# Kernel tuning notes

Measured on AMD Instinct MI355X. Metric: run time of the kernel, lower is better.

The kernel has to match this reference:

```python
import jax, jax.numpy as jnp
import numpy as np

B, H, L, D = 2, 16, 2048, 64


def setup_inputs() -> dict:
    key = jax.random.key(0)
    kq, kk, kv = jax.random.split(key, 3)
    return {
        "query": jax.random.normal(kq, (B, H, L, D), dtype=jnp.float32),
        "key": jax.random.normal(kk, (B, H, L, D), dtype=jnp.float32),
        "value": jax.random.normal(kv, (B, H, L, D), dtype=jnp.float32),
        "dhead": D,
        "causal": 1,
    }


def reference(query, key, value, dhead, causal):
    # mode='dhead': muP attention with scale 1/dhead (not 1/sqrt(dhead)).
    # Inputs/outputs in [B, H, L, D] layout (the torch code transposes to
    # [B, L, H, D] for the einsum and transposes back; net layout is the same).
    scale = 1.0 / dhead
    a = jnp.einsum('bhld,bhLd->bhlL', query, key) * scale  # [B,H,L,L]
    if causal:
        seq = a.shape[-1]
        mask = jnp.tril(jnp.ones((seq, seq), dtype=bool))  # [L,L]
        a = jnp.where(mask, a, jnp.float32(-jnp.inf))
    a = jax.nn.softmax(a, axis=-1)
    out = jnp.einsum('bhlL,bhLd->bhld', a, value)  # [B,H,L,D]
    return out
```

## Files before the change

### kernel.cpp

```cpp
#include <hip/hip_runtime.h>

#define BHH 32
#define SEQ 2048
#define DH 64
#define BQ 64
#define BK 64
#define NKT (SEQ / BK)
#define NQB (SEQ / BQ)
#define NT  (BHH * NKT)

typedef __attribute__((ext_vector_type(8))) _Float16 half8_t;
typedef __attribute__((ext_vector_type(4))) _Float16 half4_t;
typedef __attribute__((ext_vector_type(2))) _Float16 half2_t;
typedef __attribute__((ext_vector_type(4))) float f32x4;

__device__ __forceinline__ void async_copy16(const void* g, const void* lds) {
    __builtin_amdgcn_global_load_lds(
        (const __attribute__((address_space(1))) unsigned int*)g,
        (__attribute__((address_space(3))) unsigned int*)lds, 16, 0, 0);
}

__device__ __forceinline__ half2_t pkrtz(float a, float b) {
    return __builtin_bit_cast(half2_t, __builtin_amdgcn_cvt_pkrtz(a, b));
}

__global__ __launch_bounds__(256) void prep_kv(const float* __restrict__ K,
                                               const float* __restrict__ V,
                                               _Float16* __restrict__ Kf,
                                               _Float16* __restrict__ Vf) {
    __shared__ _Float16 l[64 * 76];
    const int t = threadIdx.x;
    const int wave = t >> 6, lane = t & 63, ln15 = lane & 15, quad = lane >> 4;
    const int row = t >> 2, col0 = (t & 3) * 16;
    int b = blockIdx.x;

    if (b < NT) {
        const float4* src = (const float4*)(K + (size_t)b * 4096 + row * 64 + col0);
        #pragma unroll
        for (int q = 0; q < 2; ++q) {
            float4 f0 = src[q * 2], f1 = src[q * 2 + 1];
            half8_t w = { (_Float16)f0.x, (_Float16)f0.y, (_Float16)f0.z, (_Float16)f0.w,
                          (_Float16)f1.x, (_Float16)f1.y, (_Float16)f1.z, (_Float16)f1.w };
            *(half8_t*)&l[row * 72 + col0 + q * 8] = w;
        }
        __syncthreads();
        #pragma unroll
        for (int p = 0; p < 2; ++p) {
            const int bid = wave * 2 + p, c = bid >> 1, k0 = bid & 1;
            half8_t w = *(const half8_t*)&l[(c * 16 + ln15) * 72 + k0 * 32 + quad * 8];
            *(half8_t*)&Kf[(size_t)b * 4096 + bid * 512 + lane * 8] = w;
        }
    } else {
        b -= NT;
        const float4* src = (const float4*)(V + (size_t)b * 4096 + row * 64 + col0);
        #pragma unroll
        for (int q = 0; q < 4; ++q) {
            float4 f = src[q];
            half4_t w = { (_Float16)f.x, (_Float16)f.y, (_Float16)f.z, (_Float16)f.w };
            *(half4_t*)&l[row * 76 + col0 + q * 4] = w;
        }
        __syncthreads();
        #pragma unroll
        for (int p = 0; p < 2; ++p) {
            const int f = wave * 2 + p, cn = f >> 1, k1 = f & 1;
            half8_t w;
            #pragma unroll
            for (int jj = 0; jj < 8; ++jj) {
                const int krow = k1 * 32 + ((jj & 4) << 2) + quad * 4 + (jj & 3);
                w[jj] = l[krow * 76 + cn * 16 + ln15];
            }
            *(half8_t*)&Vf[(size_t)b * 4096 + f * 512 + lane * 8] = w;
        }
    }
}

__global__ __launch_bounds__(256, 3) void fattn_kernel(
        const float* __restrict__ Q, const _Float16* __restrict__ Kf,
        const _Float16* __restrict__ Vf, float* __restrict__ O) {
    const int bh = blockIdx.x & 31;
    const int r = blockIdx.x >> 5, j = r & 7, rnd = r >> 3;
    const int qb = (rnd == 0) ? 31 - j : (rnd == 1) ? 16 + j
                 : (rnd == 2) ? 15 - j : j;
    const int tid  = threadIdx.x;
    const int wave = tid >> 6;
    const int lane = tid & 63;
    const int ln15 = lane & 15;
    const int quad = lane >> 4;

    __shared__ _Float16 ldsK[3][4096];
    __shared__ _Float16 ldsV[3][4096];

    const size_t base = (size_t)bh * SEQ * DH;
    const int q0   = qb * BQ;
    const int qrow = q0 + wave * 16;
    const size_t tb = (size_t)(bh * NKT) * 4096;

    const _Float16* gsrc = ((wave < 2) ? Kf : Vf) + tb + (wave & 1) * 2048 + lane * 8;
    _Float16* sdst0 = ((wave < 2) ? &ldsK[0][0] : &ldsV[0][0]) + (wave & 1) * 2048;

    #define STAGE(kt_, dd_) do {                                         \
        const _Float16* s_ = gsrc + (size_t)(kt_) * 4096;                \
        _Float16* d_ = (dd_);                                            \
        async_copy16(s_,        d_);                                     \
        async_copy16(s_ + 512,  d_ + 512);                               \
        async_copy16(s_ + 1024, d_ + 1024);                              \
        async_copy16(s_ + 1536, d_ + 1536);                              \
    } while (0)

    const float qscale = 1.44269504f / 64.0f;
    half8_t qfrag[2];
    {
        const float* qp = Q + base + (size_t)(qrow + ln15) * DH + quad * 8;
        #pragma unroll
        for (int k0 = 0; k0 < 2; ++k0) {
            float4 a = *(const float4*)(qp + k0 * 32);
            float4 b2 = *(const float4*)(qp + k0 * 32 + 4);
            qfrag[k0] = (half8_t){
                (_Float16)(a.x * qscale), (_Float16)(a.y * qscale),
                (_Float16)(a.z * qscale), (_Float16)(a.w * qscale),
                (_Float16)(b2.x * qscale), (_Float16)(b2.y * qscale),
                (_Float16)(b2.z * qscale), (_Float16)(b2.w * qscale) };
        }
    }
    asm volatile("" ::: "memory");

    STAGE(0, sdst0);
    STAGE(1, sdst0 + 4096);

    f32x4 acc[4] = {};
    float l_lane = 0.f;

    const _Float16* kbase = &ldsK[0][0] + lane * 8;
    const _Float16* vbase = &ldsV[0][0] + lane * 8;
    const int myrel = wave * 16 + ln15;
    const int kq4 = quad * 4;

    int bs = 0, b2 = 2;
    for (int kt = 0; kt <= qb; ++kt) {
        if (kt < qb)
            asm volatile("s_waitcnt vmcnt(4) lgkmcnt(0)\n\ts_barrier" ::: "memory");
        else
            asm volatile("s_waitcnt vmcnt(0) lgkmcnt(0)\n\ts_barrier" ::: "memory");

        if (kt + 2 <= qb) STAGE(kt + 2, sdst0 + b2 * 4096);

        const _Float16* kk = kbase + bs * 4096;
        const _Float16* vv = vbase + bs * 4096;

        f32x4 st[4];
        #pragma unroll
        for (int c = 0; c < 4; ++c) {
            half8_t kf0 = *(const half8_t*)(kk + c * 1024);
            half8_t kf1 = *(const half8_t*)(kk + c * 1024 + 512);
            f32x4 a = {};
            a = __builtin_amdgcn_mfma_f32_16x16x32_f16(kf0, qfrag[0], a, 0, 0, 0);
            a = __builtin_amdgcn_mfma_f32_16x16x32_f16(kf1, qfrag[1], a, 0, 0, 0);
            st[c] = a;
        }

        float p[4][4];
        #pragma unroll
        for (int c = 0; c < 4; ++c)
            #pragma unroll
            for (int rr = 0; rr < 4; ++rr)
                p[c][rr] = __builtin_amdgcn_exp2f(st[c][rr]);

        if (kt == qb) {
            #pragma unroll
            for (int c = 0; c < 4; ++c)
                #pragma unroll
                for (int rr = 0; rr < 4; ++rr)
                    if (c * 16 + kq4 + rr > myrel) p[c][rr] = 0.f;
        }

        float s0 = (p[0][0] + p[0][1]) + (p[0][2] + p[0][3]);
        float s1 = (p[1][0] + p[1][1]) + (p[1][2] + p[1][3]);
        float s2 = (p[2][0] + p[2][1]) + (p[2][2] + p[2][3]);
        float s3 = (p[3][0] + p[3][1]) + (p[3][2] + p[3][3]);
        l_lane += (s0 + s1) + (s2 + s3);

        union P8 { half2_t h2[4]; half8_t h8; };
        P8 u0, u1;
        u0.h2[0] = pkrtz(p[0][0], p[0][1]);
        u0.h2[1] = pkrtz(p[0][2], p[0][3]);
        u0.h2[2] = pkrtz(p[1][0], p[1][1]);
        u0.h2[3] = pkrtz(p[1][2], p[1][3]);
        u1.h2[0] = pkrtz(p[2][0], p[2][1]);
        u1.h2[1] = pkrtz(p[2][2], p[2][3]);
        u1.h2[2] = pkrtz(p[3][0], p[3][1]);
        u1.h2[3] = pkrtz(p[3][2], p[3][3]);
        half8_t pb0 = u0.h8, pb1 = u1.h8;

        __builtin_amdgcn_s_setprio(1);
        #pragma unroll
        for (int cn = 0; cn < 4; ++cn) {
            half8_t vf0 = *(const half8_t*)(vv + cn * 1024);
            acc[cn] = __builtin_amdgcn_mfma_f32_16x16x32_f16(vf0, pb0, acc[cn], 0, 0, 0);
            half8_t vf1 = *(const half8_t*)(vv + cn * 1024 + 512);
            acc[cn] = __builtin_amdgcn_mfma_f32_16x16x32_f16(vf1, pb1, acc[cn], 0, 0, 0);
        }
        __builtin_amdgcn_s_setprio(0);

        bs = (bs == 2) ? 0 : bs + 1;
        b2 = (b2 == 2) ? 0 : b2 + 1;
    }

    {
        float l_i = l_lane + __shfl_xor(l_lane, 16);
        l_i += __shfl_xor(l_i, 32);
        const float rl = 1.0f / l_i;
        float* op = O + base + (size_t)(qrow + ln15) * DH;
        #pragma unroll
        for (int cn = 0; cn < 4; ++cn) {
            float4 o;
            o.x = acc[cn][0] * rl;
            o.y = acc[cn][1] * rl;
            o.z = acc[cn][2] * rl;
            o.w = acc[cn][3] * rl;
            *(float4*)(op + cn * 16 + kq4) = o;
        }
    }
    #undef STAGE
}

extern "C" void kernel_launch(void* const* d_in, const int* in_sizes, int n_in,
                              void* d_out, int out_size, void* d_ws, size_t ws_size,
                              hipStream_t stream) {
    const float* Q = (const float*)d_in[0];
    const float* K = (const float*)d_in[1];
    const float* V = (const float*)d_in[2];
    float* O = (float*)d_out;
    _Float16* Kf = (_Float16*)d_ws;
    _Float16* Vf = Kf + (size_t)NT * 4096;
    prep_kv<<<2 * NT, 256, 0, stream>>>(K, V, Kf, Vf);
    fattn_kernel<<<NQB * BHH, 256, 0, stream>>>(Q, Kf, Vf, O);
}
```

Baseline: 122.6 us.

## Software-pipeline QK^T of next tile with softmax and PV of current tile

Restructures the causal attention loop so the QK^T MFMAs for tile kt+1 are issued before the exp/pack/PV work of tile kt, with a prologue computing the first scores and an epilogue that handles the masked diagonal tile. The intent is to let the matrix units overlap the exp2 and conversion work and hide dependency latency. It also moves to a full vmcnt(0) wait each iteration because the K of the next tile must already be resident. The cost is more live registers (stn alongside st) and a shallower effective prefetch, which could reduce occupancy or expose load latency.

```diff
diff --git a/kernel.cpp b/kernel.cpp
--- a/kernel.cpp
+++ b/kernel.cpp
@@ -126,6 +126,7 @@
 
     STAGE(0, sdst0);
     STAGE(1, sdst0 + 4096);
+    asm volatile("s_waitcnt vmcnt(0) lgkmcnt(0)\n\ts_barrier" ::: "memory");
 
     f32x4 acc[4] = {};
     float l_lane = 0.f;
@@ -135,27 +136,37 @@
     const int myrel = wave * 16 + ln15;
     const int kq4 = quad * 4;
 
-    int bs = 0, b2 = 2;
-    for (int kt = 0; kt <= qb; ++kt) {
-        if (kt < qb)
-            asm volatile("s_waitcnt vmcnt(4) lgkmcnt(0)\n\ts_barrier" ::: "memory");
-        else
+    f32x4 st[4];
+    #pragma unroll
+    for (int c = 0; c < 4; ++c) {
+        half8_t kf0 = *(const half8_t*)(kbase + c * 1024);
+        half8_t kf1 = *(const half8_t*)(kbase + c * 1024 + 512);
+        f32x4 a = {};
+        a = __builtin_amdgcn_mfma_f32_16x16x32_f16(kf0, qfrag[0], a, 0, 0, 0);
+        a = __builtin_amdgcn_mfma_f32_16x16x32_f16(kf1, qfrag[1], a, 0, 0, 0);
+        st[c] = a;
+    }
+
+    union P8 { half2_t h2[4]; half8_t h8; };
+    int rv = 0, rk = 1, sb = 2;
+
+    for (int kt = 0; kt < qb; ++kt) {
+        if (kt)
             asm volatile("s_waitcnt vmcnt(0) lgkmcnt(0)\n\ts_barrier" ::: "memory");
-
-        if (kt + 2 <= qb) STAGE(kt + 2, sdst0 + b2 * 4096);
-
-        const _Float16* kk = kbase + bs * 4096;
-        const _Float16* vv = vbase + bs * 4096;
-
-        f32x4 st[4];
-        #pragma unroll
-        for (int c = 0; c < 4; ++c) {
-            half8_t kf0 = *(const half8_t*)(kk + c * 1024);
-            half8_t kf1 = *(const half8_t*)(kk + c * 1024 + 512);
-            f32x4 a = {};
-            a = __builtin_amdgcn_mfma_f32_16x16x32_f16(kf0, qfrag[0], a, 0, 0, 0);
-            a = __builtin_amdgcn_mfma_f32_16x16x32_f16(kf1, qfrag[1], a, 0, 0, 0);
-            st[c] = a;
+        if (kt + 2 <= qb) STAGE(kt + 2, sdst0 + sb * 4096);
+
+        f32x4 stn[4];
+        {
+            const _Float16* kk = kbase + rk * 4096;
+            #pragma unroll
+            for (int c = 0; c < 4; ++c) {
+                half8_t kf0 = *(const half8_t*)(kk + c * 1024);
+                half8_t kf1 = *(const half8_t*)(kk + c * 1024 + 512);
+                f32x4 a = {};
+                a = __builtin_amdgcn_mfma_f32_16x16x32_f16(kf0, qfrag[0], a, 0, 0, 0);
+                a = __builtin_amdgcn_mfma_f32_16x16x32_f16(kf1, qfrag[1], a, 0, 0, 0);
+                stn[c] = a;
+            }
         }
 
         float p[4][4];
@@ -165,21 +176,6 @@
             for (int rr = 0; rr < 4; ++rr)
                 p[c][rr] = __builtin_amdgcn_exp2f(st[c][rr]);
 
-        if (kt == qb) {
-            #pragma unroll
-            for (int c = 0; c < 4; ++c)
-                #pragma unroll
-                for (int rr = 0; rr < 4; ++rr)
-                    if (c * 16 + kq4 + rr > myrel) p[c][rr] = 0.f;
-        }
-
-        float s0 = (p[0][0] + p[0][1]) + (p[0][2] + p[0][3]);
-        float s1 = (p[1][0] + p[1][1]) + (p[1][2] + p[1][3]);
-        float s2 = (p[2][0] + p[2][1]) + (p[2][2] + p[2][3]);
-        float s3 = (p[3][0] + p[3][1]) + (p[3][2] + p[3][3]);
-        l_lane += (s0 + s1) + (s2 + s3);
-
-        union P8 { half2_t h2[4]; half8_t h8; };
         P8 u0, u1;
         u0.h2[0] = pkrtz(p[0][0], p[0][1]);
         u0.h2[1] = pkrtz(p[0][2], p[0][3]);
@@ -191,6 +187,58 @@
         u1.h2[3] = pkrtz(p[3][2], p[3][3]);
         half8_t pb0 = u0.h8, pb1 = u1.h8;
 
+        {
+            const _Float16* vv = vbase + rv * 4096;
+            __builtin_amdgcn_s_setprio(1);
+            #pragma unroll
+            for (int cn = 0; cn < 4; ++cn) {
+                half8_t vf0 = *(const half8_t*)(vv + cn * 1024);
+                acc[cn] = __builtin_amdgcn_mfma_f32_16x16x32_f16(vf0, pb0, acc[cn], 0, 0, 0);
+                half8_t vf1 = *(const half8_t*)(vv + cn * 1024 + 512);
+                acc[cn] = __builtin_amdgcn_mfma_f32_16x16x32_f16(vf1, pb1, acc[cn], 0, 0, 0);
+            }
+            __builtin_amdgcn_s_setprio(0);
+        }
+
+        float s0 = (p[0][0] + p[0][1]) + (p[0][2] + p[0][3]);
+        float s1 = (p[1][0] + p[1][1]) + (p[1][2] + p[1][3]);
+        float s2 = (p[2][0] + p[2][1]) + (p[2][2] + p[2][3]);
+        float s3 = (p[3][0] + p[3][1]) + (p[3][2] + p[3][3]);
+        l_lane += (s0 + s1) + (s2 + s3);
+
+        #pragma unroll
+        for (int c = 0; c < 4; ++c) st[c] = stn[c];
+        rv = (rv == 2) ? 0 : rv + 1;
+        rk = (rk == 2) ? 0 : rk + 1;
+        sb = (sb == 2) ? 0 : sb + 1;
+    }
+
+    {
+        if (qb)
+            asm volatile("s_waitcnt vmcnt(0) lgkmcnt(0)\n\ts_barrier" ::: "memory");
+
+        float p[4][4];
+        #pragma unroll
+        for (int c = 0; c < 4; ++c)
+            #pragma unroll
+            for (int rr = 0; rr < 4; ++rr) {
+                float v = __builtin_amdgcn_exp2f(st[c][rr]);
+                if (c * 16 + kq4 + rr > myrel) v = 0.f;
+                p[c][rr] = v;
+            }
+
+        P8 u0, u1;
+        u0.h2[0] = pkrtz(p[0][0], p[0][1]);
+        u0.h2[1] = pkrtz(p[0][2], p[0][3]);
+        u0.h2[2] = pkrtz(p[1][0], p[1][1]);
+        u0.h2[3] = pkrtz(p[1][2], p[1][3]);
+        u1.h2[0] = pkrtz(p[2][0], p[2][1]);
+        u1.h2[1] = pkrtz(p[2][2], p[2][3]);
+        u1.h2[2] = pkrtz(p[3][0], p[3][1]);
+        u1.h2[3] = pkrtz(p[3][2], p[3][3]);
+        half8_t pb0 = u0.h8, pb1 = u1.h8;
+
+        const _Float16* vv = vbase + rv * 4096;
         __builtin_amdgcn_s_setprio(1);
         #pragma unroll
         for (int cn = 0; cn < 4; ++cn) {
@@ -201,8 +249,11 @@
         }
         __builtin_amdgcn_s_setprio(0);
 
-        bs = (bs == 2) ? 0 : bs + 1;
-        b2 = (b2 == 2) ? 0 : b2 + 1;
+        float s0 = (p[0][0] + p[0][1]) + (p[0][2] + p[0][3]);
+        float s1 = (p[1][0] + p[1][1]) + (p[1][2] + p[1][3]);
+        float s2 = (p[2][0] + p[2][1]) + (p[2][2] + p[2][3]);
+        float s3 = (p[3][0] + p[3][1]) + (p[3][2] + p[3][3]);
+        l_lane += (s0 + s1) + (s2 + s3);
     }
 
     {
```

Measured after the change: 125.3 us. 1.02x slower.
